# Kernel optimization log

Measured on AMD Instinct MI355X. Metric: run time of the kernel, lower is better.

Reference implementation:

```python
import math
import jax, jax.numpy as jnp
import numpy as np

IN_C = 256
OUT_C = 256
STYLE_DIM = 512
EPS = 1e-8
SCALE = 1.0 / math.sqrt(IN_C)          # fan_in = in_channel * k^2, k=1
MOD_SCALE = 1.0 / math.sqrt(STYLE_DIM) # EqualLinear default scale


def setup_inputs() -> dict:
    key = jax.random.key(0)
    k1, k2, k3, k4 = jax.random.split(key, 4)
    x = jax.random.normal(k1, (4, 65536, 256), dtype=jnp.float32)
    style = jax.random.normal(k2, (4, 512), dtype=jnp.float32)
    weight = jax.random.normal(k3, (1, 256, 256), dtype=jnp.float32)  # (1, in, out)
    mod_w = jax.random.normal(k4, (256, 512), dtype=jnp.float32)      # EqualLinear weight (out=in_c, in=style_dim)
    mod_b = jnp.ones((256,), dtype=jnp.float32)                        # bias_init=1
    return {"x": x, "style": style, "weight": weight, "mod_w": mod_w, "mod_b": mod_b}


def reference(x, style, weight, mod_w, mod_b):
    # style modulation via EqualLinear: F.linear(style, W*scale) + bias*lr_mul
    s = style @ (mod_w * MOD_SCALE).T + mod_b            # (b, in_c)
    s = s[:, :, None] + 1.0                              # (b, in_c, 1)
    # per-sample modulated weight
    w = SCALE * weight * s                               # (b, in_c, out_c)
    # demodulation: rsqrt over in_c
    demod = jax.lax.rsqrt(jnp.sum(w * w, axis=1) + EPS)  # (b, out_c)
    w = w * demod[:, None, :]
    # batched matmul: (b, n, in_c) x (b, in_c, out_c)
    return jnp.einsum('bnc,bco->bno', x, w)
```

## Files before the change

kernel.cpp:

```cpp
#include <hip/hip_runtime.h>
#include <hip/hip_bf16.h>
#include <math.h>

#define IN_C   256
#define OUT_C  256
#define SDIM   512
#define NROWS  65536

constexpr float EPS       = 1e-8f;
constexpr float SCALE     = 0.0625f;
constexpr float MOD_SCALE = 0.04419417382415922f;

typedef __bf16 bf16x8 __attribute__((ext_vector_type(8)));
typedef float  f32x4  __attribute__((ext_vector_type(4)));

__global__ __launch_bounds__(256) void modw_kernel(
    const float* __restrict__ style,
    const float* __restrict__ weight,
    const float* __restrict__ mod_w,
    const float* __restrict__ mod_b,
    __bf16* __restrict__ wt)
{
    const int b = blockIdx.x;
    const int t = threadIdx.x;

    __shared__ float s_lds[IN_C];
    __shared__ float demod_lds[OUT_C];

    {
        const float* st = style + b * SDIM;
        const float* mw = mod_w + t * SDIM;
        float dot = 0.f;
        #pragma unroll 4
        for (int j = 0; j < SDIM; j += 4) {
            float4 a = *(const float4*)(st + j);
            float4 w = *(const float4*)(mw + j);
            dot += a.x * w.x + a.y * w.y + a.z * w.z + a.w * w.w;
        }
        s_lds[t] = dot * MOD_SCALE + mod_b[t] + 1.0f;
    }
    __syncthreads();

    {
        float sum = 0.f;
        #pragma unroll 4
        for (int c = 0; c < IN_C; ++c) {
            float wv = SCALE * weight[c * OUT_C + t] * s_lds[c];
            sum += wv * wv;
        }
        demod_lds[t] = 1.0f / sqrtf(sum + EPS);
    }
    __syncthreads();

    {
        const float srow = SCALE * s_lds[t];
        __bf16* w_out = wt + b * (IN_C * OUT_C);
        const float* wrow = weight + t * OUT_C;
        #pragma unroll 4
        for (int o = 0; o < OUT_C; o += 4) {
            float4 wv = *(const float4*)(wrow + o);
            w_out[(o + 0) * IN_C + t] = (__bf16)(wv.x * srow * demod_lds[o + 0]);
            w_out[(o + 1) * IN_C + t] = (__bf16)(wv.y * srow * demod_lds[o + 1]);
            w_out[(o + 2) * IN_C + t] = (__bf16)(wv.z * srow * demod_lds[o + 2]);
            w_out[(o + 3) * IN_C + t] = (__bf16)(wv.w * srow * demod_lds[o + 3]);
        }
    }
}

__global__ __launch_bounds__(256, 2) void gemm_kernel(
    const float* __restrict__ x,
    const __bf16* __restrict__ wt,
    float* __restrict__ out)
{
    const int lane = threadIdx.x & 63;
    const int wid  = threadIdx.x >> 6;
    const int b    = blockIdx.x >> 8;
    const int tgrp = blockIdx.x & 255;

    const int l15 = lane & 15;
    const int kb  = (lane >> 4) * 8;

    bf16x8 bfrag[4][8];
    {
        const __bf16* wb = wt + b * (IN_C * OUT_C) + (wid * 64 + l15) * IN_C + kb;
        #pragma unroll
        for (int nt = 0; nt < 4; ++nt)
            #pragma unroll
            for (int ks = 0; ks < 8; ++ks)
                bfrag[nt][ks] = *(const bf16x8*)(wb + nt * 16 * IN_C + ks * 32);
    }

    const float* xb = x   + (size_t)b * NROWS * IN_C;
    float*       ob = out + (size_t)b * NROWS * OUT_C;

    for (int it = 0; it < 8; ++it) {
        const int m0 = (tgrp + (it << 8)) << 5;

        f32x4 acc[2][4] = {};

        #pragma unroll
        for (int ms = 0; ms < 2; ++ms) {
            const float* xr = xb + (size_t)(m0 + ms * 16 + l15) * IN_C + kb;
            #pragma unroll
            for (int ks = 0; ks < 8; ++ks) {
                float4 f0 = *(const float4*)(xr + ks * 32);
                float4 f1 = *(const float4*)(xr + ks * 32 + 4);
                bf16x8 a;
                a[0] = (__bf16)f0.x; a[1] = (__bf16)f0.y;
                a[2] = (__bf16)f0.z; a[3] = (__bf16)f0.w;
                a[4] = (__bf16)f1.x; a[5] = (__bf16)f1.y;
                a[6] = (__bf16)f1.z; a[7] = (__bf16)f1.w;
                #pragma unroll
                for (int nt = 0; nt < 4; ++nt)
                    acc[ms][nt] = __builtin_amdgcn_mfma_f32_16x16x32_bf16(
                        a, bfrag[nt][ks], acc[ms][nt], 0, 0, 0);
            }
        }

        const int r0 = (lane >> 4) * 4;
        #pragma unroll
        for (int ms = 0; ms < 2; ++ms) {
            #pragma unroll
            for (int nt = 0; nt < 4; ++nt) {
                float* orow = ob + (size_t)(m0 + ms * 16 + r0) * OUT_C
                                 + wid * 64 + nt * 16 + l15;
                #pragma unroll
                for (int r = 0; r < 4; ++r)
                    orow[(size_t)r * OUT_C] = acc[ms][nt][r];
            }
        }
    }
}

extern "C" void kernel_launch(void* const* d_in, const int* in_sizes, int n_in,
                              void* d_out, int out_size, void* d_ws, size_t ws_size,
                              hipStream_t stream) {
    const float* x      = (const float*)d_in[0];
    const float* style  = (const float*)d_in[1];
    const float* weight = (const float*)d_in[2];
    const float* mod_w  = (const float*)d_in[3];
    const float* mod_b  = (const float*)d_in[4];
    float* out = (float*)d_out;
    __bf16* wt = (__bf16*)d_ws;

    modw_kernel<<<4, 256, 0, stream>>>(style, weight, mod_w, mod_b, wt);
    gemm_kernel<<<1024, 256, 0, stream>>>(x, wt, out);
}
```

Baseline: 561.9 us.

## Retile GEMM into 128x64 output blocks with swizzled LDS weight tile

Replaces the persistent-style GEMM, where each block held all 256 output columns of the modulated weight in registers and looped over 8 row tiles, with a one-tile-per-block launch. Each of 8192 blocks computes a 128-row by 64-column output tile. It stages its 64-column weight slice in a 32 KB XOR-swizzled LDS buffer and raises the occupancy hint to 4 blocks. The aim is to cut register pressure and expose more parallelism and latency hiding. The cost is that each x row is now read by four separate blocks, one per column tile. Those blocks may land on different XCDs, so x traffic from HBM or the last-level cache can grow.

```diff
diff --git a/kernel.cpp b/kernel.cpp
--- a/kernel.cpp
+++ b/kernel.cpp
@@ -67,67 +67,72 @@
     }
 }
 
-__global__ __launch_bounds__(256, 2) void gemm_kernel(
+__global__ __launch_bounds__(256, 4) void gemm_kernel(
     const float* __restrict__ x,
     const __bf16* __restrict__ wt,
     float* __restrict__ out)
 {
-    const int lane = threadIdx.x & 63;
-    const int wid  = threadIdx.x >> 6;
-    const int b    = blockIdx.x >> 8;
-    const int tgrp = blockIdx.x & 255;
+    const int ntile = blockIdx.x & 3;
+    const int mtile = (blockIdx.x >> 2) & 511;
+    const int b     = blockIdx.x >> 11;
 
-    const int l15 = lane & 15;
-    const int kb  = (lane >> 4) * 8;
+    const int tid  = threadIdx.x;
+    const int lane = tid & 63;
+    const int wid  = tid >> 6;
+    const int l15  = lane & 15;
+    const int kb   = (lane >> 4) * 8;
 
-    bf16x8 bfrag[4][8];
+    __shared__ __bf16 blds[64 * IN_C];
+
     {
-        const __bf16* wb = wt + b * (IN_C * OUT_C) + (wid * 64 + l15) * IN_C + kb;
+        const float4* src = (const float4*)(wt + (size_t)b * (IN_C * OUT_C)
+                                               + (size_t)ntile * 64 * IN_C);
+        float4* dst = (float4*)blds;
         #pragma unroll
-        for (int nt = 0; nt < 4; ++nt)
-            #pragma unroll
-            for (int ks = 0; ks < 8; ++ks)
-                bfrag[nt][ks] = *(const bf16x8*)(wb + nt * 16 * IN_C + ks * 32);
+        for (int i = 0; i < 8; ++i) {
+            int chunk = tid + i * 256;
+            dst[chunk ^ ((chunk >> 5) & 7)] = src[chunk];
+        }
+    }
+    __syncthreads();
+
+    const float* xbase = x + ((size_t)b * NROWS + (size_t)mtile * 128 + wid * 32 + l15) * IN_C + kb;
+
+    f32x4 acc[2][4] = {};
+
+    #pragma unroll
+    for (int ks = 0; ks < 8; ++ks) {
+        bf16x8 a[2];
+        #pragma unroll
+        for (int ms = 0; ms < 2; ++ms) {
+            const float* xr = xbase + ms * 16 * IN_C + ks * 32;
+            float4 f0 = *(const float4*)(xr);
+            float4 f1 = *(const float4*)(xr + 4);
+            a[ms][0] = (__bf16)f0.x; a[ms][1] = (__bf16)f0.y;
+            a[ms][2] = (__bf16)f0.z; a[ms][3] = (__bf16)f0.w;
+            a[ms][4] = (__bf16)f1.x; a[ms][5] = (__bf16)f1.y;
+            a[ms][6] = (__bf16)f1.z; a[ms][7] = (__bf16)f1.w;
+        }
+        #pragma unroll
+        for (int nt = 0; nt < 4; ++nt) {
+            int chunk = ((nt * 16 + l15) << 5) + (ks << 2) + (kb >> 3);
+            bf16x8 bf = *(const bf16x8*)(blds + (size_t)(chunk ^ (l15 & 7)) * 8);
+            acc[0][nt] = __builtin_amdgcn_mfma_f32_16x16x32_bf16(a[0], bf, acc[0][nt], 0, 0, 0);
+            acc[1][nt] = __builtin_amdgcn_mfma_f32_16x16x32_bf16(a[1], bf, acc[1][nt], 0, 0, 0);
+        }
     }
 
-    const float* xb = x   + (size_t)b * NROWS * IN_C;
-    float*       ob = out + (size_t)b * NROWS * OUT_C;
-
-    for (int it = 0; it < 8; ++it) {
-        const int m0 = (tgrp + (it << 8)) << 5;
-
-        f32x4 acc[2][4] = {};
-
+    const int r0 = (lane >> 4) * 4;
+    float* obase = out + ((size_t)b * NROWS + (size_t)mtile * 128 + wid * 32) * OUT_C
+                       + ntile * 64;
+    #pragma unroll
+    for (int ms = 0; ms < 2; ++ms) {
         #pragma unroll
-        for (int ms = 0; ms < 2; ++ms) {
-            const float* xr = xb + (size_t)(m0 + ms * 16 + l15) * IN_C + kb;
+        for (int nt = 0; nt < 4; ++nt) {
+            float* orow = obase + (size_t)(ms * 16 + r0) * OUT_C + nt * 16 + l15;
             #pragma unroll
-            for (int ks = 0; ks < 8; ++ks) {
-                float4 f0 = *(const float4*)(xr + ks * 32);
-                float4 f1 = *(const float4*)(xr + ks * 32 + 4);
-                bf16x8 a;
-                a[0] = (__bf16)f0.x; a[1] = (__bf16)f0.y;
-                a[2] = (__bf16)f0.z; a[3] = (__bf16)f0.w;
-                a[4] = (__bf16)f1.x; a[5] = (__bf16)f1.y;
-                a[6] = (__bf16)f1.z; a[7] = (__bf16)f1.w;
-                #pragma unroll
-                for (int nt = 0; nt < 4; ++nt)
-                    acc[ms][nt] = __builtin_amdgcn_mfma_f32_16x16x32_bf16(
-                        a, bfrag[nt][ks], acc[ms][nt], 0, 0, 0);
-            }
-        }
-
-        const int r0 = (lane >> 4) * 4;
-        #pragma unroll
-        for (int ms = 0; ms < 2; ++ms) {
-            #pragma unroll
-            for (int nt = 0; nt < 4; ++nt) {
-                float* orow = ob + (size_t)(m0 + ms * 16 + r0) * OUT_C
-                                 + wid * 64 + nt * 16 + l15;
-                #pragma unroll
-                for (int r = 0; r < 4; ++r)
-                    orow[(size_t)r * OUT_C] = acc[ms][nt][r];
-            }
+            for (int r = 0; r < 4; ++r)
+                orow[(size_t)r * OUT_C] = acc[ms][nt][r];
         }
     }
 }
@@ -144,5 +149,5 @@
     __bf16* wt = (__bf16*)d_ws;
 
     modw_kernel<<<4, 256, 0, stream>>>(style, weight, mod_w, mod_b, wt);
-    gemm_kernel<<<1024, 256, 0, stream>>>(x, wt, out);
+    gemm_kernel<<<8192, 256, 0, stream>>>(x, wt, out);
 }
```

Result: slower. 584.7 us (+4.0%).
